# Optimization experiments

Measured on AMD Instinct MI355X. Metric: run time of the kernel, lower is better.

Reference implementation:

```python
import jax, jax.numpy as jnp
import numpy as np

D_MODEL = 1024
N_HEAD = 16
HEAD_DIM = D_MODEL // N_HEAD


def setup_inputs() -> dict:
    key = jax.random.key(0)
    ks = jax.random.split(key, 5)
    s_attn = 1.0 / np.sqrt(D_MODEL)
    s_proj = 1.0 / np.sqrt(D_MODEL)
    return {
        "x": jax.random.normal(ks[0], (4, 2048, D_MODEL), dtype=jnp.float32),
        "w_attn": jax.random.normal(ks[1], (D_MODEL, 3 * D_MODEL), dtype=jnp.float32) * s_attn,
        "b_attn": jax.random.normal(ks[2], (3 * D_MODEL,), dtype=jnp.float32) * 0.02,
        "w_proj": jax.random.normal(ks[3], (D_MODEL, D_MODEL), dtype=jnp.float32) * s_proj,
        "b_proj": jax.random.normal(ks[4], (D_MODEL,), dtype=jnp.float32) * 0.02,
    }


def reference(x, w_attn, b_attn, w_proj, b_proj):
    B, T, C = x.shape
    qkv = x @ w_attn + b_attn  # [B,T,3C]
    q, k, v = jnp.split(qkv, 3, axis=2)
    # [B,T,C] -> [B,H,T,Dh]
    def heads(t):
        return t.reshape(B, T, N_HEAD, HEAD_DIM).transpose(0, 2, 1, 3)
    q, k, v = heads(q), heads(k), heads(v)
    scale = 1.0 / np.sqrt(HEAD_DIM)
    att = jnp.einsum("bhqd,bhkd->bhqk", q, k) * scale
    att = jax.nn.softmax(att, axis=-1)  # NOTE: no causal mask in source
    y = jnp.einsum("bhqk,bhkd->bhqd", att, v)
    y = y.transpose(0, 2, 1, 3).reshape(B, T, C)
    return y @ w_proj + b_proj
```

## Files before the change

### kernel.cpp

```cpp
#include <hip/hip_runtime.h>
#include <hip/hip_bf16.h>
#include <cstdint>
#include <cstddef>

#define DI __device__ __forceinline__

typedef float f32x4 __attribute__((ext_vector_type(4)));
typedef short short8 __attribute__((ext_vector_type(8)));
typedef unsigned short us4 __attribute__((ext_vector_type(4)));
typedef unsigned int u32x2 __attribute__((ext_vector_type(2)));

constexpr int Bc = 4, Tc = 2048, Cc = 1024, Hc = 16, Dhc = 64;
constexpr int Mrows = Bc * Tc;
constexpr int N1 = 3 * Cc;
constexpr int K1 = Cc;

DI unsigned short f2bf(float f) {
  unsigned u = __builtin_bit_cast(unsigned, f);
  unsigned r = u + 0x7FFFu + ((u >> 16) & 1u);
  return (unsigned short)(r >> 16);
}
DI float bf2f(unsigned short h) {
  return __builtin_bit_cast(float, (unsigned)h << 16);
}
DI unsigned cvtpk(float a, float b) {
  unsigned r;
  asm("v_cvt_pk_bf16_f32 %0, %1, %2" : "=v"(r) : "v"(a), "v"(b));
  return r;
}

#define GLOAD16(gp, lp)                                                        \
  __builtin_amdgcn_global_load_lds(                                            \
      (const __attribute__((address_space(1))) void*)(gp),                     \
      (__attribute__((address_space(3))) void*)(lp), 16, 0, 0)

__global__ __launch_bounds__(256) void k_cast_x(const float* __restrict__ x,
                                                unsigned short* __restrict__ xb) {
  int i = (blockIdx.x * 256 + threadIdx.x) * 8;
  f32x4 a = *reinterpret_cast<const f32x4*>(x + i);
  f32x4 b = *reinterpret_cast<const f32x4*>(x + i + 4);
  us4 r0 = {f2bf(a[0]), f2bf(a[1]), f2bf(a[2]), f2bf(a[3])};
  us4 r1 = {f2bf(b[0]), f2bf(b[1]), f2bf(b[2]), f2bf(b[3])};
  *reinterpret_cast<us4*>(xb + i) = r0;
  *reinterpret_cast<us4*>(xb + i + 4) = r1;
}

__global__ __launch_bounds__(256) void k_transpose_bf(const float* __restrict__ w,
                                                      unsigned short* __restrict__ wT,
                                                      int Kd, int Nd) {
  __shared__ float t[64][65];
  int kb = blockIdx.y * 64, nb = blockIdx.x * 64;
  int c = threadIdx.x & 63, r4 = threadIdx.x >> 6;
#pragma unroll
  for (int it = 0; it < 16; ++it) {
    int r = it * 4 + r4;
    t[r][c] = w[(size_t)(kb + r) * Nd + nb + c];
  }
  __syncthreads();
#pragma unroll
  for (int it = 0; it < 16; ++it) {
    int r = it * 4 + r4;
    wT[(size_t)(nb + r) * Kd + kb + c] = f2bf(t[c][r]);
  }
}

__global__ __launch_bounds__(256) void k_gemm_qkv(
    const unsigned short* __restrict__ xb, const unsigned short* __restrict__ waT,
    const float* __restrict__ bias, unsigned short* __restrict__ q,
    unsigned short* __restrict__ kkp, unsigned short* __restrict__ vT) {
  __shared__ unsigned short lA[128 * 64];
  __shared__ unsigned short lB[128 * 64];
  const int tid = threadIdx.x, lane = tid & 63, wid = tid >> 6;
  const int wr = wid >> 1, wc = wid & 1;
  const int l15 = lane & 15, l4 = lane >> 4;
  const int bid = blockIdx.x;
  const int swz = (bid & 7) * 192 + (bid >> 3);
  const int rowBase = (swz / 24) * 128;
  const int colBase = (swz % 24) * 128;

  f32x4 acc[4][4] = {};

  for (int kt = 0; kt < K1 / 64; ++kt) {
    __syncthreads();
#pragma unroll
    for (int ch = 0; ch < 4; ++ch) {
      int d = wid * 4096 + ch * 1024 + lane * 16;
      int r = d >> 7;
      int cbyte = (d & 127) ^ ((r & 7) << 4);
      const unsigned short* ga = xb + (size_t)(rowBase + r) * K1 + kt * 64 + (cbyte >> 1);
      GLOAD16(ga, (char*)lA + wid * 4096 + ch * 1024);
      const unsigned short* gb = waT + (size_t)(colBase + r) * K1 + kt * 64 + (cbyte >> 1);
      GLOAD16(gb, (char*)lB + wid * 4096 + ch * 1024);
    }
    __syncthreads();
#pragma unroll
    for (int ks = 0; ks < 2; ++ks) {
      short8 af[4], bfv[4];
#pragma unroll
      for (int mf = 0; mf < 4; ++mf) {
        int r = wr * 64 + mf * 16 + l15;
        af[mf] = *reinterpret_cast<const short8*>(
            (const char*)lA + r * 128 + ((ks * 64 + (l4 << 4)) ^ ((r & 7) << 4)));
      }
#pragma unroll
      for (int nf = 0; nf < 4; ++nf) {
        int r = wc * 64 + nf * 16 + l15;
        bfv[nf] = *reinterpret_cast<const short8*>(
            (const char*)lB + r * 128 + ((ks * 64 + (l4 << 4)) ^ ((r & 7) << 4)));
      }
#pragma unroll
      for (int mf = 0; mf < 4; ++mf)
#pragma unroll
        for (int nf = 0; nf < 4; ++nf)
          acc[mf][nf] = __builtin_amdgcn_mfma_f32_16x16x32_bf16(af[mf], bfv[nf],
                                                                acc[mf][nf], 0, 0, 0);
    }
  }
  constexpr float C1 = 0.18033688011112042f;
  const int sec = colBase >> 10;
  const float qsc = (sec == 0) ? C1 : 1.0f;
#pragma unroll
  for (int nf = 0; nf < 4; ++nf) {
    int ccol = colBase + wc * 64 + nf * 16 + l15;
    float bv = bias[ccol];
    int cc = ccol & 1023;
    int h = cc >> 6, dd = cc & 63;
#pragma unroll
    for (int mf = 0; mf < 4; ++mf) {
      int r0 = rowBase + wr * 64 + mf * 16 + l4 * 4;
      f32x4 v = acc[mf][nf];
      if (sec == 2) {
        int b_ = r0 >> 11, t = r0 & 2047;
        int pair = b_ * 16 + h;
        us4 pk = {f2bf(v[0] + bv), f2bf(v[1] + bv), f2bf(v[2] + bv), f2bf(v[3] + bv)};
        *reinterpret_cast<us4*>(vT + ((size_t)pair * 64 + dd) * 2048 + t) = pk;
      } else {
        unsigned short* dst = (sec == 0) ? q : kkp;
#pragma unroll
        for (int j = 0; j < 4; ++j) {
          int r = r0 + j;
          int b_ = r >> 11, t = r & 2047;
          dst[((size_t)(b_ * 16 + h) * 2048 + t) * 64 + dd] = f2bf((v[j] + bv) * qsc);
        }
      }
    }
  }
}

__global__ __launch_bounds__(512) void k_attn(
    const unsigned short* __restrict__ q, const unsigned short* __restrict__ kkp,
    const unsigned short* __restrict__ vT, unsigned short* __restrict__ yb) {
  __shared__ unsigned short lK[2][64 * 64];
  __shared__ unsigned short lV[2][64 * 64];
  __shared__ unsigned short lP[8][32 * 64];
  const int tid = threadIdx.x, lane = tid & 63, wid = tid >> 6;
  const int l15 = lane & 15, l4 = lane >> 4;
  const int bid = blockIdx.x;
  const int swz = (bid & 7) * 64 + (bid >> 3);
  const int qb = swz & 7, pair = swz >> 3;
  const size_t base = (size_t)pair * Tc * Dhc;
  const int swzl = (l15 & 7) << 4;

  const int sd = wid * 1024 + lane * 16;
  const int sr = sd >> 7;
  const int scb = (sd & 127) ^ ((sr & 7) << 4);
  const unsigned short* gkbase = kkp + base + (size_t)sr * 64 + (scb >> 1);
  const unsigned short* gvbase = vT + base + (size_t)sr * 2048 + (scb >> 1);

  short8 qf[2][2];
#pragma unroll
  for (int qt = 0; qt < 2; ++qt) {
    int qrow = qb * 256 + wid * 32 + qt * 16 + l15;
#pragma unroll
    for (int ks = 0; ks < 2; ++ks)
      qf[qt][ks] = *reinterpret_cast<const short8*>(q + base + (size_t)qrow * 64 +
                                                    ks * 32 + l4 * 8);
  }

  f32x4 yac[2][4] = {};
  float lsum[2] = {0.f, 0.f};
  char* lPw = (char*)lP[wid];

  GLOAD16(gkbase, (char*)lK[0] + wid * 1024);
  GLOAD16(gvbase, (char*)lV[0] + wid * 1024);

  for (int kb = 0; kb < Tc / 64; ++kb) {
    const int b = kb & 1;
    asm volatile("s_waitcnt vmcnt(0)" ::: "memory");
    __builtin_amdgcn_s_barrier();
    if (kb < Tc / 64 - 1) {
      GLOAD16(gkbase + (size_t)(kb + 1) * 4096, (char*)lK[b ^ 1] + wid * 1024);
      GLOAD16(gvbase + (kb + 1) * 64, (char*)lV[b ^ 1] + wid * 1024);
    }

    const char* lKb = (const char*)lK[b];
#pragma unroll
    for (int nf = 0; nf < 4; ++nf) {
      int r = nf * 16 + l15;
      f32x4 s0 = {0.f, 0.f, 0.f, 0.f}, s1 = {0.f, 0.f, 0.f, 0.f};
      __builtin_amdgcn_s_setprio(1);
#pragma unroll
      for (int ks = 0; ks < 2; ++ks) {
        short8 kf = *reinterpret_cast<const short8*>(
            lKb + r * 128 + ((ks * 64 + (l4 << 4)) ^ swzl));
        s0 = __builtin_amdgcn_mfma_f32_16x16x32_bf16(kf, qf[0][ks], s0, 0, 0, 0);
        s1 = __builtin_amdgcn_mfma_f32_16x16x32_bf16(kf, qf[1][ks], s1, 0, 0, 0);
      }
      __builtin_amdgcn_s_setprio(0);
      float p0 = __builtin_amdgcn_exp2f(s0[0]);
      float p1 = __builtin_amdgcn_exp2f(s0[1]);
      float p2 = __builtin_amdgcn_exp2f(s0[2]);
      float p3 = __builtin_amdgcn_exp2f(s0[3]);
      lsum[0] += (p0 + p1) + (p2 + p3);
      u32x2 w0 = {cvtpk(p0, p1), cvtpk(p2, p3)};
      *reinterpret_cast<u32x2*>(lPw + l15 * 128 + ((nf * 32 + l4 * 8) ^ swzl)) = w0;
      p0 = __builtin_amdgcn_exp2f(s1[0]);
      p1 = __builtin_amdgcn_exp2f(s1[1]);
      p2 = __builtin_amdgcn_exp2f(s1[2]);
      p3 = __builtin_amdgcn_exp2f(s1[3]);
      lsum[1] += (p0 + p1) + (p2 + p3);
      u32x2 w1 = {cvtpk(p0, p1), cvtpk(p2, p3)};
      *reinterpret_cast<u32x2*>(lPw + (16 + l15) * 128 + ((nf * 32 + l4 * 8) ^ swzl)) = w1;
    }
    const char* lVb = (const char*)lV[b];
    __builtin_amdgcn_s_setprio(1);
#pragma unroll
    for (int ks = 0; ks < 2; ++ks) {
      short8 pf0 = *reinterpret_cast<const short8*>(
          lPw + l15 * 128 + ((ks * 64 + (l4 << 4)) ^ swzl));
      short8 pf1 = *reinterpret_cast<const short8*>(
          lPw + (16 + l15) * 128 + ((ks * 64 + (l4 << 4)) ^ swzl));
#pragma unroll
      for (int mf = 0; mf < 4; ++mf) {
        int r = mf * 16 + l15;
        short8 vf = *reinterpret_cast<const short8*>(
            lVb + r * 128 + ((ks * 64 + (l4 << 4)) ^ swzl));
        yac[0][mf] = __builtin_amdgcn_mfma_f32_16x16x32_bf16(vf, pf0, yac[0][mf], 0, 0, 0);
        yac[1][mf] = __builtin_amdgcn_mfma_f32_16x16x32_bf16(vf, pf1, yac[1][mf], 0, 0, 0);
      }
    }
    __builtin_amdgcn_s_setprio(0);
  }
  const int b_ = pair >> 4, h = pair & 15;
#pragma unroll
  for (int qt = 0; qt < 2; ++qt) {
    float l = lsum[qt];
    l += __shfl_xor(l, 16);
    l += __shfl_xor(l, 32);
    float invl = 1.0f / l;
    size_t rowg = (size_t)(b_ * 2048 + qb * 256 + wid * 32 + qt * 16 + l15);
#pragma unroll
    for (int mf = 0; mf < 4; ++mf) {
      f32x4 v = yac[qt][mf];
      us4 hi = {f2bf(v[0] * invl), f2bf(v[1] * invl), f2bf(v[2] * invl),
                f2bf(v[3] * invl)};
      size_t off = rowg * 1024 + h * 64 + mf * 16 + l4 * 4;
      *reinterpret_cast<us4*>(yb + off) = hi;
    }
  }
}

__global__ __launch_bounds__(256) void k_gemm_proj(
    const unsigned short* __restrict__ yb, const unsigned short* __restrict__ wpT,
    const float* __restrict__ bias, float* __restrict__ out) {
  __shared__ unsigned short lA[128 * 64];
  __shared__ unsigned short lB[128 * 64];
  const int tid = threadIdx.x, lane = tid & 63, wid = tid >> 6;
  const int wr = wid >> 1, wc = wid & 1;
  const int l15 = lane & 15, l4 = lane >> 4;
  const int bid = blockIdx.x;
  const int swz = (bid & 7) * 64 + (bid >> 3);
  const int rowBase = (swz >> 3) * 128;
  const int colBase = (swz & 7) * 128;

  f32x4 acc[4][4] = {};

  for (int kt = 0; kt < 16; ++kt) {
    __syncthreads();
#pragma unroll
    for (int ch = 0; ch < 4; ++ch) {
      int d = wid * 4096 + ch * 1024 + lane * 16;
      int r = d >> 7;
      int cbyte = (d & 127) ^ ((r & 7) << 4);
      const unsigned short* ga = yb + (size_t)(rowBase + r) * Cc + kt * 64 + (cbyte >> 1);
      GLOAD16(ga, (char*)lA + wid * 4096 + ch * 1024);
      const unsigned short* gb = wpT + (size_t)(colBase + r) * Cc + kt * 64 + (cbyte >> 1);
      GLOAD16(gb, (char*)lB + wid * 4096 + ch * 1024);
    }
    __syncthreads();
#pragma unroll
    for (int ks = 0; ks < 2; ++ks) {
      short8 af[4], bfv[4];
#pragma unroll
      for (int mf = 0; mf < 4; ++mf) {
        int r = wr * 64 + mf * 16 + l15;
        af[mf] = *reinterpret_cast<const short8*>(
            (const char*)lA + r * 128 + ((ks * 64 + (l4 << 4)) ^ ((r & 7) << 4)));
      }
#pragma unroll
      for (int nf = 0; nf < 4; ++nf) {
        int r = wc * 64 + nf * 16 + l15;
        bfv[nf] = *reinterpret_cast<const short8*>(
            (const char*)lB + r * 128 + ((ks * 64 + (l4 << 4)) ^ ((r & 7) << 4)));
      }
#pragma unroll
      for (int mf = 0; mf < 4; ++mf)
#pragma unroll
        for (int nf = 0; nf < 4; ++nf)
          acc[mf][nf] = __builtin_amdgcn_mfma_f32_16x16x32_bf16(af[mf], bfv[nf],
                                                                acc[mf][nf], 0, 0, 0);
    }
  }
#pragma unroll
  for (int nf = 0; nf < 4; ++nf) {
    int c = colBase + wc * 64 + nf * 16 + l15;
    float bv = bias[c];
#pragma unroll
    for (int mf = 0; mf < 4; ++mf) {
      int r0 = rowBase + wr * 64 + mf * 16 + l4 * 4;
      f32x4 v = acc[mf][nf];
#pragma unroll
      for (int j = 0; j < 4; ++j) out[(size_t)(r0 + j) * Cc + c] = v[j] + bv;
    }
  }
}

extern "C" void kernel_launch(void* const* d_in, const int* in_sizes, int n_in,
                              void* d_out, int out_size, void* d_ws, size_t ws_size,
                              hipStream_t stream) {
  const float* x = (const float*)d_in[0];
  const float* w_attn = (const float*)d_in[1];
  const float* b_attn = (const float*)d_in[2];
  const float* w_proj = (const float*)d_in[3];
  const float* b_proj = (const float*)d_in[4];
  float* out = (float*)d_out;
  char* ws = (char*)d_ws;
  const size_t MiB = 1u << 20;
  unsigned short* xb = (unsigned short*)(ws + 0 * MiB);
  unsigned short* waT = (unsigned short*)(ws + 16 * MiB);
  unsigned short* q = (unsigned short*)(ws + 22 * MiB);
  unsigned short* kk = (unsigned short*)(ws + 38 * MiB);
  unsigned short* vT = (unsigned short*)(ws + 54 * MiB);
  unsigned short* yb = (unsigned short*)(ws + 70 * MiB);
  unsigned short* wpT = (unsigned short*)(ws + 86 * MiB);

  k_cast_x<<<dim3(4096), dim3(256), 0, stream>>>(x, xb);
  k_transpose_bf<<<dim3(48, 16), dim3(256), 0, stream>>>(w_attn, waT, K1, N1);
  k_transpose_bf<<<dim3(16, 16), dim3(256), 0, stream>>>(w_proj, wpT, Cc, Cc);
  k_gemm_qkv<<<dim3(1536), dim3(256), 0, stream>>>(xb, waT, b_attn, q, kk, vT);
  k_attn<<<dim3(512), dim3(512), 0, stream>>>(q, kk, vT, yb);
  k_gemm_proj<<<dim3(512), dim3(256), 0, stream>>>(yb, wpT, b_proj, out);
}
```

Measured before the change: 261.7 us.

## Use 32x32 MFMA with register-resident P in attention; fuse prep kernels

The attention kernel moves from 16x16x32 to 32x32x16 bf16 MFMA. The softmax probabilities are repacked in registers with permlane32_swap, so the per-wave LDS round-trip for P goes away. Block size drops to 256 threads with 128 query rows per block and twice as many blocks, and each wave loads two K/V chunks per stage. The cast and two weight-transpose kernels are merged into one launch to cut launch overhead. In exchange, the larger accumulators raise register pressure, which may lower occupancy.

```diff
diff --git a/kernel.cpp b/kernel.cpp
--- a/kernel.cpp
+++ b/kernel.cpp
@@ -6,9 +6,11 @@
 #define DI __device__ __forceinline__
 
 typedef float f32x4 __attribute__((ext_vector_type(4)));
+typedef float f32x16 __attribute__((ext_vector_type(16)));
 typedef short short8 __attribute__((ext_vector_type(8)));
 typedef unsigned short us4 __attribute__((ext_vector_type(4)));
 typedef unsigned int u32x2 __attribute__((ext_vector_type(2)));
+typedef unsigned int u32x4 __attribute__((ext_vector_type(4)));
 
 constexpr int Bc = 4, Tc = 2048, Cc = 1024, Hc = 16, Dhc = 64;
 constexpr int Mrows = Bc * Tc;
@@ -28,28 +30,43 @@
   asm("v_cvt_pk_bf16_f32 %0, %1, %2" : "=v"(r) : "v"(a), "v"(b));
   return r;
 }
+DI void plswap(unsigned& x, unsigned& y) {
+  u32x2 r = __builtin_amdgcn_permlane32_swap(x, y, false, false);
+  x = r[0];
+  y = r[1];
+}
 
 #define GLOAD16(gp, lp)                                                        \
   __builtin_amdgcn_global_load_lds(                                            \
       (const __attribute__((address_space(1))) void*)(gp),                     \
       (__attribute__((address_space(3))) void*)(lp), 16, 0, 0)
 
-__global__ __launch_bounds__(256) void k_cast_x(const float* __restrict__ x,
-                                                unsigned short* __restrict__ xb) {
-  int i = (blockIdx.x * 256 + threadIdx.x) * 8;
-  f32x4 a = *reinterpret_cast<const f32x4*>(x + i);
-  f32x4 b = *reinterpret_cast<const f32x4*>(x + i + 4);
-  us4 r0 = {f2bf(a[0]), f2bf(a[1]), f2bf(a[2]), f2bf(a[3])};
-  us4 r1 = {f2bf(b[0]), f2bf(b[1]), f2bf(b[2]), f2bf(b[3])};
-  *reinterpret_cast<us4*>(xb + i) = r0;
-  *reinterpret_cast<us4*>(xb + i + 4) = r1;
-}
-
-__global__ __launch_bounds__(256) void k_transpose_bf(const float* __restrict__ w,
-                                                      unsigned short* __restrict__ wT,
-                                                      int Kd, int Nd) {
+__global__ __launch_bounds__(256) void k_prep(
+    const float* __restrict__ x, unsigned short* __restrict__ xb,
+    const float* __restrict__ w_attn, unsigned short* __restrict__ waT,
+    const float* __restrict__ w_proj, unsigned short* __restrict__ wpT) {
   __shared__ float t[64][65];
-  int kb = blockIdx.y * 64, nb = blockIdx.x * 64;
+  const int bid = blockIdx.x;
+  if (bid < 4096) {
+    int i = (bid * 256 + threadIdx.x) * 8;
+    f32x4 a = *reinterpret_cast<const f32x4*>(x + i);
+    f32x4 b = *reinterpret_cast<const f32x4*>(x + i + 4);
+    us4 r0 = {f2bf(a[0]), f2bf(a[1]), f2bf(a[2]), f2bf(a[3])};
+    us4 r1 = {f2bf(b[0]), f2bf(b[1]), f2bf(b[2]), f2bf(b[3])};
+    *reinterpret_cast<us4*>(xb + i) = r0;
+    *reinterpret_cast<us4*>(xb + i + 4) = r1;
+    return;
+  }
+  const float* w;
+  unsigned short* wT;
+  int Kd, Nd, idx;
+  if (bid < 4096 + 768) {
+    idx = bid - 4096; w = w_attn; wT = waT; Kd = 1024; Nd = 3072;
+  } else {
+    idx = bid - 4864; w = w_proj; wT = wpT; Kd = 1024; Nd = 1024;
+  }
+  int nx = (Nd == 3072) ? 48 : 16;
+  int nb = (idx % nx) * 64, kb = (idx / nx) * 64;
   int c = threadIdx.x & 63, r4 = threadIdx.x >> 6;
 #pragma unroll
   for (int it = 0; it < 16; ++it) {
@@ -147,115 +164,118 @@
   }
 }
 
-__global__ __launch_bounds__(512) void k_attn(
+__global__ __launch_bounds__(256) void k_attn(
     const unsigned short* __restrict__ q, const unsigned short* __restrict__ kkp,
     const unsigned short* __restrict__ vT, unsigned short* __restrict__ yb) {
   __shared__ unsigned short lK[2][64 * 64];
   __shared__ unsigned short lV[2][64 * 64];
-  __shared__ unsigned short lP[8][32 * 64];
   const int tid = threadIdx.x, lane = tid & 63, wid = tid >> 6;
-  const int l15 = lane & 15, l4 = lane >> 4;
+  const int l31 = lane & 31, hf = lane >> 5;
   const int bid = blockIdx.x;
-  const int swz = (bid & 7) * 64 + (bid >> 3);
-  const int qb = swz & 7, pair = swz >> 3;
+  const int swz = (bid & 7) * 128 + (bid >> 3);
+  const int qb = swz & 15, pair = swz >> 4;
   const size_t base = (size_t)pair * Tc * Dhc;
-  const int swzl = (l15 & 7) << 4;
-
-  const int sd = wid * 1024 + lane * 16;
-  const int sr = sd >> 7;
-  const int scb = (sd & 127) ^ ((sr & 7) << 4);
-  const unsigned short* gkbase = kkp + base + (size_t)sr * 64 + (scb >> 1);
-  const unsigned short* gvbase = vT + base + (size_t)sr * 2048 + (scb >> 1);
-
-  short8 qf[2][2];
-#pragma unroll
-  for (int qt = 0; qt < 2; ++qt) {
-    int qrow = qb * 256 + wid * 32 + qt * 16 + l15;
-#pragma unroll
-    for (int ks = 0; ks < 2; ++ks)
-      qf[qt][ks] = *reinterpret_cast<const short8*>(q + base + (size_t)qrow * 64 +
-                                                    ks * 32 + l4 * 8);
-  }
-
-  f32x4 yac[2][4] = {};
-  float lsum[2] = {0.f, 0.f};
-  char* lPw = (char*)lP[wid];
-
-  GLOAD16(gkbase, (char*)lK[0] + wid * 1024);
-  GLOAD16(gvbase, (char*)lV[0] + wid * 1024);
+  const int rswz = (l31 & 7) << 4;
+
+  const int sd0 = wid * 2048 + lane * 16;
+  const int sr0 = sd0 >> 7;
+  const int sc0 = (sd0 & 127) ^ ((sr0 & 7) << 4);
+  const int sd1 = sd0 + 1024;
+  const int sr1 = sd1 >> 7;
+  const int sc1 = (sd1 & 127) ^ ((sr1 & 7) << 4);
+  const unsigned short* gk0 = kkp + base + (size_t)sr0 * 64 + (sc0 >> 1);
+  const unsigned short* gk1 = kkp + base + (size_t)sr1 * 64 + (sc1 >> 1);
+  const unsigned short* gv0 = vT + base + (size_t)sr0 * 2048 + (sc0 >> 1);
+  const unsigned short* gv1 = vT + base + (size_t)sr1 * 2048 + (sc1 >> 1);
+
+  short8 qf[4];
+  const int qrow = qb * 128 + wid * 32 + l31;
+#pragma unroll
+  for (int ks = 0; ks < 4; ++ks)
+    qf[ks] = *reinterpret_cast<const short8*>(q + base + (size_t)qrow * 64 +
+                                              ks * 16 + hf * 8);
+
+  f32x16 yac[2] = {};
+  float lsum = 0.f;
+
+  GLOAD16(gk0, (char*)lK[0] + wid * 2048);
+  GLOAD16(gk1, (char*)lK[0] + wid * 2048 + 1024);
+  GLOAD16(gv0, (char*)lV[0] + wid * 2048);
+  GLOAD16(gv1, (char*)lV[0] + wid * 2048 + 1024);
 
   for (int kb = 0; kb < Tc / 64; ++kb) {
     const int b = kb & 1;
     asm volatile("s_waitcnt vmcnt(0)" ::: "memory");
     __builtin_amdgcn_s_barrier();
     if (kb < Tc / 64 - 1) {
-      GLOAD16(gkbase + (size_t)(kb + 1) * 4096, (char*)lK[b ^ 1] + wid * 1024);
-      GLOAD16(gvbase + (kb + 1) * 64, (char*)lV[b ^ 1] + wid * 1024);
+      const size_t ka = (size_t)(kb + 1) * 4096;
+      const int va = (kb + 1) * 64;
+      GLOAD16(gk0 + ka, (char*)lK[b ^ 1] + wid * 2048);
+      GLOAD16(gk1 + ka, (char*)lK[b ^ 1] + wid * 2048 + 1024);
+      GLOAD16(gv0 + va, (char*)lV[b ^ 1] + wid * 2048);
+      GLOAD16(gv1 + va, (char*)lV[b ^ 1] + wid * 2048 + 1024);
     }
 
     const char* lKb = (const char*)lK[b];
-#pragma unroll
-    for (int nf = 0; nf < 4; ++nf) {
-      int r = nf * 16 + l15;
-      f32x4 s0 = {0.f, 0.f, 0.f, 0.f}, s1 = {0.f, 0.f, 0.f, 0.f};
+    const char* lVb = (const char*)lV[b];
+    short8 pf[2][2];
+#pragma unroll
+    for (int kt2 = 0; kt2 < 2; ++kt2) {
+      f32x16 s = {};
       __builtin_amdgcn_s_setprio(1);
 #pragma unroll
-      for (int ks = 0; ks < 2; ++ks) {
+      for (int ks = 0; ks < 4; ++ks) {
         short8 kf = *reinterpret_cast<const short8*>(
-            lKb + r * 128 + ((ks * 64 + (l4 << 4)) ^ swzl));
-        s0 = __builtin_amdgcn_mfma_f32_16x16x32_bf16(kf, qf[0][ks], s0, 0, 0, 0);
-        s1 = __builtin_amdgcn_mfma_f32_16x16x32_bf16(kf, qf[1][ks], s1, 0, 0, 0);
+            lKb + (kt2 * 32 + l31) * 128 + ((ks * 32 + hf * 16) ^ rswz));
+        s = __builtin_amdgcn_mfma_f32_32x32x16_bf16(kf, qf[ks], s, 0, 0, 0);
       }
       __builtin_amdgcn_s_setprio(0);
-      float p0 = __builtin_amdgcn_exp2f(s0[0]);
-      float p1 = __builtin_amdgcn_exp2f(s0[1]);
-      float p2 = __builtin_amdgcn_exp2f(s0[2]);
-      float p3 = __builtin_amdgcn_exp2f(s0[3]);
-      lsum[0] += (p0 + p1) + (p2 + p3);
-      u32x2 w0 = {cvtpk(p0, p1), cvtpk(p2, p3)};
-      *reinterpret_cast<u32x2*>(lPw + l15 * 128 + ((nf * 32 + l4 * 8) ^ swzl)) = w0;
-      p0 = __builtin_amdgcn_exp2f(s1[0]);
-      p1 = __builtin_amdgcn_exp2f(s1[1]);
-      p2 = __builtin_amdgcn_exp2f(s1[2]);
-      p3 = __builtin_amdgcn_exp2f(s1[3]);
-      lsum[1] += (p0 + p1) + (p2 + p3);
-      u32x2 w1 = {cvtpk(p0, p1), cvtpk(p2, p3)};
-      *reinterpret_cast<u32x2*>(lPw + (16 + l15) * 128 + ((nf * 32 + l4 * 8) ^ swzl)) = w1;
-    }
-    const char* lVb = (const char*)lV[b];
+      float p[16];
+#pragma unroll
+      for (int r = 0; r < 16; ++r) p[r] = __builtin_amdgcn_exp2f(s[r]);
+#pragma unroll
+      for (int r = 0; r < 16; ++r) lsum += p[r];
+      unsigned a0 = cvtpk(p[0], p[1]), a1 = cvtpk(p[2], p[3]);
+      unsigned c0 = cvtpk(p[4], p[5]), c1 = cvtpk(p[6], p[7]);
+      plswap(a0, c0);
+      plswap(a1, c1);
+      u32x4 w0 = {a0, a1, c0, c1};
+      pf[kt2][0] = __builtin_bit_cast(short8, w0);
+      unsigned d0 = cvtpk(p[8], p[9]), d1 = cvtpk(p[10], p[11]);
+      unsigned e0 = cvtpk(p[12], p[13]), e1 = cvtpk(p[14], p[15]);
+      plswap(d0, e0);
+      plswap(d1, e1);
+      u32x4 w1 = {d0, d1, e0, e1};
+      pf[kt2][1] = __builtin_bit_cast(short8, w1);
+    }
     __builtin_amdgcn_s_setprio(1);
 #pragma unroll
-    for (int ks = 0; ks < 2; ++ks) {
-      short8 pf0 = *reinterpret_cast<const short8*>(
-          lPw + l15 * 128 + ((ks * 64 + (l4 << 4)) ^ swzl));
-      short8 pf1 = *reinterpret_cast<const short8*>(
-          lPw + (16 + l15) * 128 + ((ks * 64 + (l4 << 4)) ^ swzl));
-#pragma unroll
-      for (int mf = 0; mf < 4; ++mf) {
-        int r = mf * 16 + l15;
-        short8 vf = *reinterpret_cast<const short8*>(
-            lVb + r * 128 + ((ks * 64 + (l4 << 4)) ^ swzl));
-        yac[0][mf] = __builtin_amdgcn_mfma_f32_16x16x32_bf16(vf, pf0, yac[0][mf], 0, 0, 0);
-        yac[1][mf] = __builtin_amdgcn_mfma_f32_16x16x32_bf16(vf, pf1, yac[1][mf], 0, 0, 0);
-      }
-    }
+    for (int dt = 0; dt < 2; ++dt)
+#pragma unroll
+      for (int kt2 = 0; kt2 < 2; ++kt2)
+#pragma unroll
+        for (int kw = 0; kw < 2; ++kw) {
+          short8 vf = *reinterpret_cast<const short8*>(
+              lVb + (dt * 32 + l31) * 128 +
+              ((kt2 * 64 + kw * 32 + hf * 16) ^ rswz));
+          yac[dt] = __builtin_amdgcn_mfma_f32_32x32x16_bf16(vf, pf[kt2][kw],
+                                                            yac[dt], 0, 0, 0);
+        }
     __builtin_amdgcn_s_setprio(0);
   }
-  const int b_ = pair >> 4, h = pair & 15;
-#pragma unroll
-  for (int qt = 0; qt < 2; ++qt) {
-    float l = lsum[qt];
-    l += __shfl_xor(l, 16);
-    l += __shfl_xor(l, 32);
-    float invl = 1.0f / l;
-    size_t rowg = (size_t)(b_ * 2048 + qb * 256 + wid * 32 + qt * 16 + l15);
-#pragma unroll
-    for (int mf = 0; mf < 4; ++mf) {
-      f32x4 v = yac[qt][mf];
-      us4 hi = {f2bf(v[0] * invl), f2bf(v[1] * invl), f2bf(v[2] * invl),
-                f2bf(v[3] * invl)};
-      size_t off = rowg * 1024 + h * 64 + mf * 16 + l4 * 4;
-      *reinterpret_cast<us4*>(yb + off) = hi;
+  lsum += __shfl_xor(lsum, 32);
+  float invl = 1.0f / lsum;
+  const int b_ = pair >> 4, hh = pair & 15;
+  const size_t rowg = (size_t)(b_ * 2048 + qb * 128 + wid * 32 + l31);
+#pragma unroll
+  for (int dt = 0; dt < 2; ++dt) {
+    f32x16 Y = yac[dt];
+#pragma unroll
+    for (int qd = 0; qd < 4; ++qd) {
+      us4 o = {f2bf(Y[qd * 4 + 0] * invl), f2bf(Y[qd * 4 + 1] * invl),
+               f2bf(Y[qd * 4 + 2] * invl), f2bf(Y[qd * 4 + 3] * invl)};
+      int col = hh * 64 + dt * 32 + qd * 8 + hf * 4;
+      *reinterpret_cast<us4*>(yb + rowg * 1024 + col) = o;
     }
   }
 }
@@ -344,10 +364,8 @@
   unsigned short* yb = (unsigned short*)(ws + 70 * MiB);
   unsigned short* wpT = (unsigned short*)(ws + 86 * MiB);
 
-  k_cast_x<<<dim3(4096), dim3(256), 0, stream>>>(x, xb);
-  k_transpose_bf<<<dim3(48, 16), dim3(256), 0, stream>>>(w_attn, waT, K1, N1);
-  k_transpose_bf<<<dim3(16, 16), dim3(256), 0, stream>>>(w_proj, wpT, Cc, Cc);
+  k_prep<<<dim3(5120), dim3(256), 0, stream>>>(x, xb, w_attn, waT, w_proj, wpT);
   k_gemm_qkv<<<dim3(1536), dim3(256), 0, stream>>>(xb, waT, b_attn, q, kk, vT);
-  k_attn<<<dim3(512), dim3(512), 0, stream>>>(q, kk, vT, yb);
+  k_attn<<<dim3(1024), dim3(256), 0, stream>>>(q, kk, vT, yb);
   k_gemm_proj<<<dim3(512), dim3(256), 0, stream>>>(yb, wpT, b_proj, out);
 }
```

After: 280.0 us. 7.0% more time.

## Keep attention P in registers via permlane swaps; merge prep kernels into one launch

Applied to the files above, without the earlier changes.

The attention kernel no longer stages the softmax probabilities through a per-wave LDS buffer. It rearranges the packed bf16 P values across lanes with permlane32/permlane16 swaps so they form the MFMA B-operand fragments directly. This removes the LDS writes and reads for P, and the LDS footprint that may limit occupancy, at the cost of extra cross-lane permute instructions. Separately, the cast and the two weight-transpose kernels are merged into a single launch with block-index dispatch, which removes two kernel launches.

```diff
diff --git a/kernel.cpp b/kernel.cpp
--- a/kernel.cpp
+++ b/kernel.cpp
@@ -9,6 +9,7 @@
 typedef short short8 __attribute__((ext_vector_type(8)));
 typedef unsigned short us4 __attribute__((ext_vector_type(4)));
 typedef unsigned int u32x2 __attribute__((ext_vector_type(2)));
+typedef unsigned int u32x4 __attribute__((ext_vector_type(4)));
 
 constexpr int Bc = 4, Tc = 2048, Cc = 1024, Hc = 16, Dhc = 64;
 constexpr int Mrows = Bc * Tc;
@@ -28,28 +29,48 @@
   asm("v_cvt_pk_bf16_f32 %0, %1, %2" : "=v"(r) : "v"(a), "v"(b));
   return r;
 }
+DI void plswap32(unsigned& x, unsigned& y) {
+  u32x2 r = __builtin_amdgcn_permlane32_swap(x, y, false, false);
+  x = r[0];
+  y = r[1];
+}
+DI void plswap16(unsigned& x, unsigned& y) {
+  u32x2 r = __builtin_amdgcn_permlane16_swap(x, y, false, false);
+  x = r[0];
+  y = r[1];
+}
 
 #define GLOAD16(gp, lp)                                                        \
   __builtin_amdgcn_global_load_lds(                                            \
       (const __attribute__((address_space(1))) void*)(gp),                     \
       (__attribute__((address_space(3))) void*)(lp), 16, 0, 0)
 
-__global__ __launch_bounds__(256) void k_cast_x(const float* __restrict__ x,
-                                                unsigned short* __restrict__ xb) {
-  int i = (blockIdx.x * 256 + threadIdx.x) * 8;
-  f32x4 a = *reinterpret_cast<const f32x4*>(x + i);
-  f32x4 b = *reinterpret_cast<const f32x4*>(x + i + 4);
-  us4 r0 = {f2bf(a[0]), f2bf(a[1]), f2bf(a[2]), f2bf(a[3])};
-  us4 r1 = {f2bf(b[0]), f2bf(b[1]), f2bf(b[2]), f2bf(b[3])};
-  *reinterpret_cast<us4*>(xb + i) = r0;
-  *reinterpret_cast<us4*>(xb + i + 4) = r1;
-}
-
-__global__ __launch_bounds__(256) void k_transpose_bf(const float* __restrict__ w,
-                                                      unsigned short* __restrict__ wT,
-                                                      int Kd, int Nd) {
+__global__ __launch_bounds__(256) void k_prep(
+    const float* __restrict__ x, unsigned short* __restrict__ xb,
+    const float* __restrict__ w_attn, unsigned short* __restrict__ waT,
+    const float* __restrict__ w_proj, unsigned short* __restrict__ wpT) {
   __shared__ float t[64][65];
-  int kb = blockIdx.y * 64, nb = blockIdx.x * 64;
+  const int bid = blockIdx.x;
+  if (bid < 4096) {
+    int i = (bid * 256 + threadIdx.x) * 8;
+    f32x4 a = *reinterpret_cast<const f32x4*>(x + i);
+    f32x4 b = *reinterpret_cast<const f32x4*>(x + i + 4);
+    us4 r0 = {f2bf(a[0]), f2bf(a[1]), f2bf(a[2]), f2bf(a[3])};
+    us4 r1 = {f2bf(b[0]), f2bf(b[1]), f2bf(b[2]), f2bf(b[3])};
+    *reinterpret_cast<us4*>(xb + i) = r0;
+    *reinterpret_cast<us4*>(xb + i + 4) = r1;
+    return;
+  }
+  const float* w;
+  unsigned short* wT;
+  int Kd, Nd, idx;
+  if (bid < 4096 + 768) {
+    idx = bid - 4096; w = w_attn; wT = waT; Kd = 1024; Nd = 3072;
+  } else {
+    idx = bid - 4864; w = w_proj; wT = wpT; Kd = 1024; Nd = 1024;
+  }
+  int nx = (Nd == 3072) ? 48 : 16;
+  int nb = (idx % nx) * 64, kb = (idx / nx) * 64;
   int c = threadIdx.x & 63, r4 = threadIdx.x >> 6;
 #pragma unroll
   for (int it = 0; it < 16; ++it) {
@@ -152,7 +173,6 @@
     const unsigned short* __restrict__ vT, unsigned short* __restrict__ yb) {
   __shared__ unsigned short lK[2][64 * 64];
   __shared__ unsigned short lV[2][64 * 64];
-  __shared__ unsigned short lP[8][32 * 64];
   const int tid = threadIdx.x, lane = tid & 63, wid = tid >> 6;
   const int l15 = lane & 15, l4 = lane >> 4;
   const int bid = blockIdx.x;
@@ -172,14 +192,13 @@
   for (int qt = 0; qt < 2; ++qt) {
     int qrow = qb * 256 + wid * 32 + qt * 16 + l15;
 #pragma unroll
-    for (int ks = 0; ks < 2; ++ks)
-      qf[qt][ks] = *reinterpret_cast<const short8*>(q + base + (size_t)qrow * 64 +
-                                                    ks * 32 + l4 * 8);
+    for (int kd = 0; kd < 2; ++kd)
+      qf[qt][kd] = *reinterpret_cast<const short8*>(q + base + (size_t)qrow * 64 +
+                                                    kd * 32 + l4 * 8);
   }
 
   f32x4 yac[2][4] = {};
   float lsum[2] = {0.f, 0.f};
-  char* lPw = (char*)lP[wid];
 
   GLOAD16(gkbase, (char*)lK[0] + wid * 1024);
   GLOAD16(gvbase, (char*)lV[0] + wid * 1024);
@@ -194,49 +213,62 @@
     }
 
     const char* lKb = (const char*)lK[b];
-#pragma unroll
-    for (int nf = 0; nf < 4; ++nf) {
-      int r = nf * 16 + l15;
-      f32x4 s0 = {0.f, 0.f, 0.f, 0.f}, s1 = {0.f, 0.f, 0.f, 0.f};
-      __builtin_amdgcn_s_setprio(1);
-#pragma unroll
-      for (int ks = 0; ks < 2; ++ks) {
-        short8 kf = *reinterpret_cast<const short8*>(
-            lKb + r * 128 + ((ks * 64 + (l4 << 4)) ^ swzl));
-        s0 = __builtin_amdgcn_mfma_f32_16x16x32_bf16(kf, qf[0][ks], s0, 0, 0, 0);
-        s1 = __builtin_amdgcn_mfma_f32_16x16x32_bf16(kf, qf[1][ks], s1, 0, 0, 0);
-      }
-      __builtin_amdgcn_s_setprio(0);
-      float p0 = __builtin_amdgcn_exp2f(s0[0]);
-      float p1 = __builtin_amdgcn_exp2f(s0[1]);
-      float p2 = __builtin_amdgcn_exp2f(s0[2]);
-      float p3 = __builtin_amdgcn_exp2f(s0[3]);
-      lsum[0] += (p0 + p1) + (p2 + p3);
-      u32x2 w0 = {cvtpk(p0, p1), cvtpk(p2, p3)};
-      *reinterpret_cast<u32x2*>(lPw + l15 * 128 + ((nf * 32 + l4 * 8) ^ swzl)) = w0;
-      p0 = __builtin_amdgcn_exp2f(s1[0]);
-      p1 = __builtin_amdgcn_exp2f(s1[1]);
-      p2 = __builtin_amdgcn_exp2f(s1[2]);
-      p3 = __builtin_amdgcn_exp2f(s1[3]);
-      lsum[1] += (p0 + p1) + (p2 + p3);
-      u32x2 w1 = {cvtpk(p0, p1), cvtpk(p2, p3)};
-      *reinterpret_cast<u32x2*>(lPw + (16 + l15) * 128 + ((nf * 32 + l4 * 8) ^ swzl)) = w1;
-    }
     const char* lVb = (const char*)lV[b];
+    short8 pf[2][2];
+#pragma unroll
+    for (int w = 0; w < 2; ++w) {
+      unsigned wrd[2][2][2];
+#pragma unroll
+      for (int nfh = 0; nfh < 2; ++nfh) {
+        const int nf = 2 * w + nfh;
+        const int r = nf * 16 + l15;
+        f32x4 s0 = {0.f, 0.f, 0.f, 0.f}, s1 = {0.f, 0.f, 0.f, 0.f};
+        __builtin_amdgcn_s_setprio(1);
+#pragma unroll
+        for (int kd = 0; kd < 2; ++kd) {
+          short8 kf = *reinterpret_cast<const short8*>(
+              lKb + r * 128 + ((kd * 64 + (l4 << 4)) ^ swzl));
+          s0 = __builtin_amdgcn_mfma_f32_16x16x32_bf16(kf, qf[0][kd], s0, 0, 0, 0);
+          s1 = __builtin_amdgcn_mfma_f32_16x16x32_bf16(kf, qf[1][kd], s1, 0, 0, 0);
+        }
+        __builtin_amdgcn_s_setprio(0);
+        float p0 = __builtin_amdgcn_exp2f(s0[0]);
+        float p1 = __builtin_amdgcn_exp2f(s0[1]);
+        float p2 = __builtin_amdgcn_exp2f(s0[2]);
+        float p3 = __builtin_amdgcn_exp2f(s0[3]);
+        lsum[0] += (p0 + p1) + (p2 + p3);
+        wrd[0][nfh][0] = cvtpk(p0, p1);
+        wrd[0][nfh][1] = cvtpk(p2, p3);
+        p0 = __builtin_amdgcn_exp2f(s1[0]);
+        p1 = __builtin_amdgcn_exp2f(s1[1]);
+        p2 = __builtin_amdgcn_exp2f(s1[2]);
+        p3 = __builtin_amdgcn_exp2f(s1[3]);
+        lsum[1] += (p0 + p1) + (p2 + p3);
+        wrd[1][nfh][0] = cvtpk(p0, p1);
+        wrd[1][nfh][1] = cvtpk(p2, p3);
+      }
+#pragma unroll
+      for (int qt = 0; qt < 2; ++qt) {
+        unsigned u0 = wrd[qt][0][0], v0 = wrd[qt][1][0];
+        plswap32(u0, v0);
+        plswap16(u0, v0);
+        unsigned u1 = wrd[qt][0][1], v1 = wrd[qt][1][1];
+        plswap32(u1, v1);
+        plswap16(u1, v1);
+        u32x4 fr = {u0, u1, v0, v1};
+        pf[qt][w] = __builtin_bit_cast(short8, fr);
+      }
+    }
     __builtin_amdgcn_s_setprio(1);
 #pragma unroll
-    for (int ks = 0; ks < 2; ++ks) {
-      short8 pf0 = *reinterpret_cast<const short8*>(
-          lPw + l15 * 128 + ((ks * 64 + (l4 << 4)) ^ swzl));
-      short8 pf1 = *reinterpret_cast<const short8*>(
-          lPw + (16 + l15) * 128 + ((ks * 64 + (l4 << 4)) ^ swzl));
+    for (int w = 0; w < 2; ++w) {
 #pragma unroll
       for (int mf = 0; mf < 4; ++mf) {
         int r = mf * 16 + l15;
         short8 vf = *reinterpret_cast<const short8*>(
-            lVb + r * 128 + ((ks * 64 + (l4 << 4)) ^ swzl));
-        yac[0][mf] = __builtin_amdgcn_mfma_f32_16x16x32_bf16(vf, pf0, yac[0][mf], 0, 0, 0);
-        yac[1][mf] = __builtin_amdgcn_mfma_f32_16x16x32_bf16(vf, pf1, yac[1][mf], 0, 0, 0);
+            lVb + r * 128 + ((w * 64 + (l4 << 4)) ^ swzl));
+        yac[0][mf] = __builtin_amdgcn_mfma_f32_16x16x32_bf16(vf, pf[0][w], yac[0][mf], 0, 0, 0);
+        yac[1][mf] = __builtin_amdgcn_mfma_f32_16x16x32_bf16(vf, pf[1][w], yac[1][mf], 0, 0, 0);
       }
     }
     __builtin_amdgcn_s_setprio(0);
@@ -344,9 +376,7 @@
   unsigned short* yb = (unsigned short*)(ws + 70 * MiB);
   unsigned short* wpT = (unsigned short*)(ws + 86 * MiB);
 
-  k_cast_x<<<dim3(4096), dim3(256), 0, stream>>>(x, xb);
-  k_transpose_bf<<<dim3(48, 16), dim3(256), 0, stream>>>(w_attn, waT, K1, N1);
-  k_transpose_bf<<<dim3(16, 16), dim3(256), 0, stream>>>(w_proj, wpT, Cc, Cc);
+  k_prep<<<dim3(5120), dim3(256), 0, stream>>>(x, xb, w_attn, waT, w_proj, wpT);
   k_gemm_qkv<<<dim3(1536), dim3(256), 0, stream>>>(xb, waT, b_attn, q, kk, vT);
   k_attn<<<dim3(512), dim3(512), 0, stream>>>(q, kk, vT, yb);
   k_gemm_proj<<<dim3(512), dim3(256), 0, stream>>>(yb, wpT, b_proj, out);
```

Result: slower. 268.1 us (+2.5%).
